# Kernel tuning notes

Measured on AMD Instinct MI355X. Metric: run time of the kernel, lower is better.

Reference implementation:

```python
import jax, jax.numpy as jnp
import numpy as np

M = 768   # num edges
N = 768   # num loops (== M because original tiles image_x with len(edge_x) for both)
C = 256
IMG = 1024
CAT = 3 * C + IMG  # 1792, 'sharing' suffix without '1d'/'noimage'
EPS = 1e-4


def _lin_block(x, W, b):
    # LinearBlock: Linear + ReLU
    return jax.nn.relu(x @ W + b)


def _pred_head(x, W1, b1, W2, b2):
    # Sequential(LinearBlock(256,64), Linear(64,1)) -> sigmoid -> flatten
    return jax.nn.sigmoid(_lin_block(x, W1, b1) @ W2 + b2).reshape(-1)


def setup_inputs() -> dict:
    key = jax.random.key(0)
    ks = jax.random.split(key, 24)
    s = 0.02
    return {
        "edge_x": jax.random.normal(ks[0], (M, C), jnp.float32),
        "loop_x": jax.random.normal(ks[1], (N, C), jnp.float32),
        "image_x": jax.random.normal(ks[2], (1, IMG), jnp.float32),
        "loop_edge_masks": (jax.random.uniform(ks[3], (N, M)) < 0.3).astype(jnp.float32),
        "edge_conflict_mask": (jax.random.uniform(ks[4], (M, M)) < 0.1).astype(jnp.float32),
        "loop_conflict_mask": (jax.random.uniform(ks[5], (N, N)) < 0.1).astype(jnp.float32),
        "loop_masks": jax.random.uniform(ks[6], (N, 64), jnp.float32),      # pass-through only
        "loop_edge_indices": jax.random.randint(ks[7], (N,), 0, M, jnp.int32),  # unused ('1d' off)
        "edge_info": jax.random.normal(ks[8], (M, 4), jnp.float32),         # unused ('1d' off)
        "W_e3": jax.random.normal(ks[9], (CAT, C), jnp.float32) * s,
        "b_e3": jnp.zeros((C,), jnp.float32),
        "W_l3": jax.random.normal(ks[10], (CAT, C), jnp.float32) * s,
        "b_l3": jnp.zeros((C,), jnp.float32),
        "W_ep1": jax.random.normal(ks[11], (C, 64), jnp.float32) * s,
        "b_ep1": jnp.zeros((64,), jnp.float32),
        "W_ep2": jax.random.normal(ks[12], (64, 1), jnp.float32) * s,
        "b_ep2": jnp.zeros((1,), jnp.float32),
        "W_lp1": jax.random.normal(ks[13], (C, 64), jnp.float32) * s,
        "b_lp1": jnp.zeros((64,), jnp.float32),
        "W_lp2": jax.random.normal(ks[14], (64, 1), jnp.float32) * s,
        "b_lp2": jnp.zeros((1,), jnp.float32),
    }


def reference(edge_x, loop_x, image_x, loop_edge_masks, edge_conflict_mask,
              loop_conflict_mask, loop_masks, loop_edge_indices, edge_info,
              W_e3, b_e3, W_l3, b_l3, W_ep1, b_ep1, W_ep2, b_ep2,
              W_lp1, b_lp1, W_lp2, b_lp2):
    # iteration-0 predictions (appended to results in original)
    e0 = _pred_head(edge_x, W_ep1, b_ep1, W_ep2, b_ep2)  # [M]
    l0 = _pred_head(loop_x, W_lp1, b_lp1, W_lp2, b_lp2)  # [N]

    # weights[n, m] = mask * |loop_pred[n] - edge_pred[m]|
    w = loop_edge_masks * jnp.abs(l0[:, None] - e0[None, :])  # [N, M]

    # weighted broadcast sums (einsum == unsqueeze-multiply-sum in the original)
    edge_x_from_loop = jnp.einsum('nm,nc->mc', w, loop_x) \
        / jnp.maximum(w.sum(0), EPS)[:, None]               # [M, C]
    loop_x_from_edge = jnp.einsum('nm,mc->nc', w, edge_x) \
        / jnp.maximum(w.sum(1), EPS)[:, None]               # [N, C]

    # conflict-masked max pooling (materializes [M,M,C]/[N,N,C] like the original)
    edge_x_from_conflict = jnp.max(edge_conflict_mask[:, :, None] * edge_x[None, :, :], axis=1)
    loop_x_from_conflict = jnp.max(loop_conflict_mask[:, :, None] * loop_x[None, :, :], axis=1)

    img_e = jnp.broadcast_to(image_x, (edge_x.shape[0], image_x.shape[1]))
    img_l = jnp.broadcast_to(image_x, (loop_x.shape[0], image_x.shape[1]))

    edge_x2 = _lin_block(jnp.concatenate([edge_x, edge_x_from_loop, edge_x_from_conflict, img_e], axis=-1), W_e3, b_e3)
    loop_x2 = _lin_block(jnp.concatenate([loop_x, loop_x_from_edge, loop_x_from_conflict, img_l], axis=-1), W_l3, b_l3)

    e1 = _pred_head(edge_x2, W_ep1, b_ep1, W_ep2, b_ep2)
    l1 = _pred_head(loop_x2, W_lp1, b_lp1, W_lp2, b_lp2)

    # original returns results=[[e0,l0,masks,loop_masks],[e1,l1,masks,loop_masks]];
    # masks are constant pass-throughs, so we return the predictions concatenated.
    return jnp.concatenate([e0, l0, e1, l1])  # [2*(M+N)] = [3072]
```

## Files before the change

### kernel.cpp

```cpp
#include <hip/hip_runtime.h>
#include <hip/hip_bf16.h>
#include <math.h>

#define MM 768
#define CC 256
#define EPSV 1e-4f

__device__ __forceinline__ float sigmoidf_(float x) { return 1.0f / (1.0f + expf(-x)); }

__global__ __launch_bounds__(256) void k_prep(
    const float* __restrict__ edge_x, const float* __restrict__ loop_x,
    const float* __restrict__ image_x,
    const float* __restrict__ ecm, const float* __restrict__ lcm,
    const float* __restrict__ We3, const float* __restrict__ Wl3,
    const float* __restrict__ Wep1, const float* __restrict__ bep1,
    const float* __restrict__ Wep2, const float* __restrict__ bep2,
    const float* __restrict__ Wlp1, const float* __restrict__ blp1,
    const float* __restrict__ Wlp2, const float* __restrict__ blp2,
    float* __restrict__ out, float* __restrict__ efc, float* __restrict__ lfc,
    float* __restrict__ imgpart)
{
    int bid = blockIdx.x;
    int t   = threadIdx.x;

    if (bid < 1536) {
        __shared__ int   s_cnt;
        __shared__ int   s_idx[MM];
        __shared__ float s_val[MM];
        bool isLoop = bid >= MM;
        int  m      = bid & (MM - 1);
        const float* mask = isLoop ? lcm : ecm;
        const float* x    = isLoop ? loop_x : edge_x;
        float*       o    = isLoop ? lfc : efc;

        if (t == 0) s_cnt = 0;
        __syncthreads();
        int lane = t & 63;
        #pragma unroll
        for (int r = 0; r < 3; ++r) {
            int j = t + r * 256;
            float v = mask[m * MM + j];
            bool nz = (v != 0.0f);
            unsigned long long b = __ballot(nz);
            int prefix = __popcll(b & ((1ull << lane) - 1ull));
            int cntw   = __popcll(b);
            int base = 0;
            if (lane == 0 && cntw) base = atomicAdd(&s_cnt, cntw);
            base = __shfl(base, 0, 64);
            if (nz) { s_idx[base + prefix] = j; s_val[base + prefix] = v; }
        }
        __syncthreads();
        int cnt = s_cnt;
        float init = (cnt < MM) ? 0.0f : -INFINITY;
        float a0 = init, a1 = init, a2 = init, a3 = init;
        int i = 0;
        for (; i + 4 <= cnt; i += 4) {
            a0 = fmaxf(a0, s_val[i + 0] * x[s_idx[i + 0] * CC + t]);
            a1 = fmaxf(a1, s_val[i + 1] * x[s_idx[i + 1] * CC + t]);
            a2 = fmaxf(a2, s_val[i + 2] * x[s_idx[i + 2] * CC + t]);
            a3 = fmaxf(a3, s_val[i + 3] * x[s_idx[i + 3] * CC + t]);
        }
        for (; i < cnt; ++i)
            a0 = fmaxf(a0, s_val[i] * x[s_idx[i] * CC + t]);
        o[m * CC + t] = fmaxf(fmaxf(a0, a1), fmaxf(a2, a3));

    } else if (bid < 1920) {
        int wave = t >> 6, lane = t & 63;
        int row  = (bid - 1536) * 4 + wave;
        const float *x, *W1, *b1, *W2;
        float b2v;
        if (row < MM) { x = edge_x + row * CC;        W1 = Wep1; b1 = bep1; W2 = Wep2; b2v = bep2[0]; }
        else          { x = loop_x + (row - MM) * CC; W1 = Wlp1; b1 = blp1; W2 = Wlp2; b2v = blp2[0]; }

        float a0 = 0.f, a1 = 0.f, a2 = 0.f, a3 = 0.f;
        for (int cc = 0; cc < CC; cc += 4) {
            float4 xv = *reinterpret_cast<const float4*>(x + cc);
            a0 = fmaf(xv.x, W1[(cc + 0) * 64 + lane], a0);
            a1 = fmaf(xv.y, W1[(cc + 1) * 64 + lane], a1);
            a2 = fmaf(xv.z, W1[(cc + 2) * 64 + lane], a2);
            a3 = fmaf(xv.w, W1[(cc + 3) * 64 + lane], a3);
        }
        float h = fmaxf(b1[lane] + ((a0 + a1) + (a2 + a3)), 0.0f);
        float p = h * W2[lane];
        #pragma unroll
        for (int off = 32; off; off >>= 1) p += __shfl_xor(p, off, 64);
        if (lane == 0) out[row] = sigmoidf_(p + b2v);

    } else {
        int sub   = bid - 1920;
        int chunk = sub & 3;
        int head  = sub >> 2;
        const float* W = head ? Wl3 : We3;
        int k0 = chunk * 256;
        float s = 0.0f;
        #pragma unroll 4
        for (int k = 0; k < 256; ++k)
            s = fmaf(image_x[k0 + k], W[(768 + k0 + k) * CC + t], s);
        imgpart[head * 1024 + chunk * 256 + t] = s;
    }
}

__global__ __launch_bounds__(512) void k_bsum(
    const float* __restrict__ lem, const float* __restrict__ edge_x,
    const float* __restrict__ loop_x, const float* __restrict__ pred,
    float* __restrict__ efl, float* __restrict__ lfe)
{
    __shared__ float4 s_wv4[MM];
    __shared__ float  s_pw[8 * 4];
    __shared__ float  s_sum[4];
    float* s_wv = reinterpret_cast<float*>(s_wv4);

    int bid = blockIdx.x;
    int t   = threadIdx.x;
    const float* e0 = pred;
    const float* l0 = pred + MM;

    bool isE = bid < 192;
    int  r0  = (isE ? bid : bid - 192) * 4;
    const float* ownp = isE ? e0 : l0;
    const float* othp = isE ? l0 : e0;

    float own[4];
    #pragma unroll
    for (int i = 0; i < 4; ++i) own[i] = ownp[r0 + i];

    int i_ = t & 3;
    float myown = own[0];
    if (i_ == 1) myown = own[1];
    else if (i_ == 2) myown = own[2];
    else if (i_ == 3) myown = own[3];
    float psum = 0.f;
    #pragma unroll
    for (int k = 0; k < 6; ++k) {
        int idx = t + k * 512;
        int s = idx >> 2;
        float lm = isE ? lem[s * MM + r0 + i_] : lem[(r0 + i_) * MM + s];
        float wv = lm * fabsf(othp[s] - myown);
        s_wv[idx] = wv;
        psum += wv;
    }
    #pragma unroll
    for (int off = 4; off < 64; off <<= 1) psum += __shfl_xor(psum, off, 64);
    int wave = t >> 6, lane = t & 63;
    if (lane < 4) s_pw[wave * 4 + lane] = psum;
    __syncthreads();
    if (t < 4) {
        float s = 0.f;
        #pragma unroll
        for (int w = 0; w < 8; ++w) s += s_pw[w * 4 + t];
        s_sum[t] = fmaxf(s, EPSV);
    }

    const float* xsrc = isE ? loop_x : edge_x;
    int c = t & 255, h = t >> 8;
    float acc0 = 0.f, acc1 = 0.f, acc2 = 0.f, acc3 = 0.f;
    int s0 = h * 384;
    for (int s = s0; s < s0 + 384; s += 4) {
        float4 wa = s_wv4[s + 0];
        float4 wb = s_wv4[s + 1];
        float4 wc = s_wv4[s + 2];
        float4 wd = s_wv4[s + 3];
        float xa = xsrc[(s + 0) * CC + c];
        float xb = xsrc[(s + 1) * CC + c];
        float xc = xsrc[(s + 2) * CC + c];
        float xd = xsrc[(s + 3) * CC + c];
        acc0 = fmaf(wa.x, xa, acc0); acc1 = fmaf(wa.y, xa, acc1);
        acc2 = fmaf(wa.z, xa, acc2); acc3 = fmaf(wa.w, xa, acc3);
        acc0 = fmaf(wb.x, xb, acc0); acc1 = fmaf(wb.y, xb, acc1);
        acc2 = fmaf(wb.z, xb, acc2); acc3 = fmaf(wb.w, xb, acc3);
        acc0 = fmaf(wc.x, xc, acc0); acc1 = fmaf(wc.y, xc, acc1);
        acc2 = fmaf(wc.z, xc, acc2); acc3 = fmaf(wc.w, xc, acc3);
        acc0 = fmaf(wd.x, xd, acc0); acc1 = fmaf(wd.y, xd, acc1);
        acc2 = fmaf(wd.z, xd, acc2); acc3 = fmaf(wd.w, xd, acc3);
    }
    __syncthreads();
    if (h == 1) {
        s_wv[0 * CC + c] = acc0; s_wv[1 * CC + c] = acc1;
        s_wv[2 * CC + c] = acc2; s_wv[3 * CC + c] = acc3;
    }
    __syncthreads();
    if (h == 0) {
        float* outp = isE ? efl : lfe;
        outp[(r0 + 0) * CC + c] = (acc0 + s_wv[0 * CC + c]) / s_sum[0];
        outp[(r0 + 1) * CC + c] = (acc1 + s_wv[1 * CC + c]) / s_sum[1];
        outp[(r0 + 2) * CC + c] = (acc2 + s_wv[2 * CC + c]) / s_sum[2];
        outp[(r0 + 3) * CC + c] = (acc3 + s_wv[3 * CC + c]) / s_sum[3];
    }
}

__global__ __launch_bounds__(512) void k_cat(
    const float* __restrict__ edge_x, const float* __restrict__ loop_x,
    const float* __restrict__ efl, const float* __restrict__ lfe,
    const float* __restrict__ efc, const float* __restrict__ lfc,
    const float* __restrict__ We3, const float* __restrict__ be3,
    const float* __restrict__ Wl3, const float* __restrict__ bl3,
    const float* __restrict__ imgpart,
    const float* __restrict__ Wep1, const float* __restrict__ bep1,
    const float* __restrict__ Wep2, const float* __restrict__ bep2,
    const float* __restrict__ Wlp1, const float* __restrict__ blp1,
    const float* __restrict__ Wlp2, const float* __restrict__ blp2,
    float* __restrict__ out)
{
    __shared__ float s_part[4 * CC];
    __shared__ float s_act[4 * CC];
    __shared__ float s_h[8 * 64];

    int head = blockIdx.y;
    const float* W  = head ? Wl3 : We3;
    const float* b  = head ? bl3 : be3;
    const float* x0 = head ? loop_x : edge_x;
    const float* x1 = head ? lfe : efl;
    const float* x2 = head ? lfc : efc;
    const float* ip = imgpart + head * 1024;

    int m0 = blockIdx.x * 4;
    int t  = threadIdx.x;
    int c  = t & 255, h = t >> 8;

    float acc[4] = {0.f, 0.f, 0.f, 0.f};

    auto accum = [&](const float* src, int ks, int kw, int len) {
        for (int kk = 0; kk < len; kk += 4) {
            float4 xv[4];
            #pragma unroll
            for (int i = 0; i < 4; ++i)
                xv[i] = *reinterpret_cast<const float4*>(src + (m0 + i) * CC + ks + kk);
            #pragma unroll
            for (int j = 0; j < 4; ++j) {
                float wv = W[(kw + kk + j) * CC + c];
                #pragma unroll
                for (int i = 0; i < 4; ++i)
                    acc[i] = fmaf(reinterpret_cast<const float*>(&xv[i])[j], wv, acc[i]);
            }
        }
    };
    if (h == 0) { accum(x0, 0, 0, 256);     accum(x1, 0, 256, 128); }
    else        { accum(x1, 128, 384, 128); accum(x2, 0, 512, 256); }

    if (h == 1) {
        #pragma unroll
        for (int i = 0; i < 4; ++i) s_part[i * CC + c] = acc[i];
    }
    __syncthreads();
    if (h == 0) {
        float bias = b[c] + ip[c] + ip[256 + c] + ip[512 + c] + ip[768 + c];
        #pragma unroll
        for (int i = 0; i < 4; ++i)
            s_act[i * CC + c] = fmaxf(bias + acc[i] + s_part[i * CC + c], 0.0f);
    }
    __syncthreads();

    int wave = t >> 6, lane = t & 63;
    int row = wave >> 1, khalf = wave & 1;
    const float* W1 = head ? Wlp1 : Wep1;
    const float* b1 = head ? blp1 : bep1;
    const float* W2 = head ? Wlp2 : Wep2;
    float b2v       = head ? blp2[0] : bep2[0];
    const float* xr = s_act + row * CC + khalf * 128;

    float a0 = 0.f, a1 = 0.f, a2 = 0.f, a3 = 0.f;
    for (int cc = 0; cc < 128; cc += 4) {
        float4 xv = *reinterpret_cast<const float4*>(xr + cc);
        int kb = khalf * 128 + cc;
        a0 = fmaf(xv.x, W1[(kb + 0) * 64 + lane], a0);
        a1 = fmaf(xv.y, W1[(kb + 1) * 64 + lane], a1);
        a2 = fmaf(xv.z, W1[(kb + 2) * 64 + lane], a2);
        a3 = fmaf(xv.w, W1[(kb + 3) * 64 + lane], a3);
    }
    s_h[wave * 64 + lane] = (a0 + a1) + (a2 + a3);
    __syncthreads();
    if (khalf == 0) {
        float hv = fmaxf(b1[lane] + s_h[wave * 64 + lane] + s_h[(wave + 1) * 64 + lane], 0.0f);
        float p = hv * W2[lane];
        #pragma unroll
        for (int off = 32; off; off >>= 1) p += __shfl_xor(p, off, 64);
        if (lane == 0) out[1536 + head * MM + m0 + row] = sigmoidf_(p + b2v);
    }
}

extern "C" void kernel_launch(void* const* d_in, const int* in_sizes, int n_in,
                              void* d_out, int out_size, void* d_ws, size_t ws_size,
                              hipStream_t stream)
{
    const float* edge_x  = (const float*)d_in[0];
    const float* loop_x  = (const float*)d_in[1];
    const float* image_x = (const float*)d_in[2];
    const float* lem     = (const float*)d_in[3];
    const float* ecm     = (const float*)d_in[4];
    const float* lcm     = (const float*)d_in[5];
    const float* We3  = (const float*)d_in[9];
    const float* be3  = (const float*)d_in[10];
    const float* Wl3  = (const float*)d_in[11];
    const float* bl3  = (const float*)d_in[12];
    const float* Wep1 = (const float*)d_in[13];
    const float* bep1 = (const float*)d_in[14];
    const float* Wep2 = (const float*)d_in[15];
    const float* bep2 = (const float*)d_in[16];
    const float* Wlp1 = (const float*)d_in[17];
    const float* blp1 = (const float*)d_in[18];
    const float* Wlp2 = (const float*)d_in[19];
    const float* blp2 = (const float*)d_in[20];

    float* out = (float*)d_out;
    float* ws  = (float*)d_ws;

    float* imgpart = ws;
    float* efl     = ws + 2048;
    float* lfe     = efl + MM * CC;
    float* efc     = lfe + MM * CC;
    float* lfc     = efc + MM * CC;

    k_prep<<<1928, 256, 0, stream>>>(edge_x, loop_x, image_x, ecm, lcm,
                                     We3, Wl3,
                                     Wep1, bep1, Wep2, bep2,
                                     Wlp1, blp1, Wlp2, blp2,
                                     out, efc, lfc, imgpart);

    k_bsum<<<384, 512, 0, stream>>>(lem, edge_x, loop_x, out, efl, lfe);

    k_cat<<<dim3(192, 2), 512, 0, stream>>>(edge_x, loop_x, efl, lfe, efc, lfc,
                                            We3, be3, Wl3, bl3, imgpart,
                                            Wep1, bep1, Wep2, bep2,
                                            Wlp1, blp1, Wlp2, blp2, out);
}
```

Measured before the change: 169.9 us.

## Split-K the bsum matmul across two blocks and register-tile both GEMM kernels

k_bsum now runs two blocks per 4-row group. Each block recomputes the full weight vector and its normalizer, but accumulates only half of the source rows. It writes a partial, already-normalized result into a separate buffer, and k_cat adds the two partials when it loads them. Both k_bsum and k_cat switch from one output column per thread with split halves to 8 waves, each covering a slice of K, with float4 loads and a 4x4 register tile per thread. The per-wave partials are combined by a shared-memory tree reduction. This aims for better occupancy and vectorized memory access, at the cost of duplicated weight-vector work, extra workspace traffic for the partials, and several extra barriers.

```diff
diff --git a/kernel.cpp b/kernel.cpp
--- a/kernel.cpp
+++ b/kernel.cpp
@@ -103,32 +103,31 @@
 __global__ __launch_bounds__(512) void k_bsum(
     const float* __restrict__ lem, const float* __restrict__ edge_x,
     const float* __restrict__ loop_x, const float* __restrict__ pred,
-    float* __restrict__ efl, float* __restrict__ lfe)
+    float* __restrict__ efl_p0, float* __restrict__ efl_p1,
+    float* __restrict__ lfe_p0, float* __restrict__ lfe_p1)
 {
     __shared__ float4 s_wv4[MM];
     __shared__ float  s_pw[8 * 4];
     __shared__ float  s_sum[4];
+    __shared__ float  s_red[4 * 16 * 64];
     float* s_wv = reinterpret_cast<float*>(s_wv4);
 
-    int bid = blockIdx.x;
-    int t   = threadIdx.x;
+    int bid  = blockIdx.x;
+    int t    = threadIdx.x;
+    int pair = bid >> 1, sh = bid & 1;
     const float* e0 = pred;
     const float* l0 = pred + MM;
 
-    bool isE = bid < 192;
-    int  r0  = (isE ? bid : bid - 192) * 4;
+    bool isE = pair < 192;
+    int  r0  = (isE ? pair : pair - 192) * 4;
     const float* ownp = isE ? e0 : l0;
     const float* othp = isE ? l0 : e0;
 
-    float own[4];
-    #pragma unroll
-    for (int i = 0; i < 4; ++i) own[i] = ownp[r0 + i];
+    float own0 = ownp[r0], own1 = ownp[r0 + 1], own2 = ownp[r0 + 2], own3 = ownp[r0 + 3];
 
     int i_ = t & 3;
-    float myown = own[0];
-    if (i_ == 1) myown = own[1];
-    else if (i_ == 2) myown = own[2];
-    else if (i_ == 3) myown = own[3];
+    float myown = own0;
+    if (i_ == 1) myown = own1; else if (i_ == 2) myown = own2; else if (i_ == 3) myown = own3;
     float psum = 0.f;
     #pragma unroll
     for (int k = 0; k < 6; ++k) {
@@ -152,45 +151,87 @@
     }
 
     const float* xsrc = isE ? loop_x : edge_x;
-    int c = t & 255, h = t >> 8;
-    float acc0 = 0.f, acc1 = 0.f, acc2 = 0.f, acc3 = 0.f;
-    int s0 = h * 384;
-    for (int s = s0; s < s0 + 384; s += 4) {
-        float4 wa = s_wv4[s + 0];
-        float4 wb = s_wv4[s + 1];
-        float4 wc = s_wv4[s + 2];
-        float4 wd = s_wv4[s + 3];
-        float xa = xsrc[(s + 0) * CC + c];
-        float xb = xsrc[(s + 1) * CC + c];
-        float xc = xsrc[(s + 2) * CC + c];
-        float xd = xsrc[(s + 3) * CC + c];
-        acc0 = fmaf(wa.x, xa, acc0); acc1 = fmaf(wa.y, xa, acc1);
-        acc2 = fmaf(wa.z, xa, acc2); acc3 = fmaf(wa.w, xa, acc3);
-        acc0 = fmaf(wb.x, xb, acc0); acc1 = fmaf(wb.y, xb, acc1);
-        acc2 = fmaf(wb.z, xb, acc2); acc3 = fmaf(wb.w, xb, acc3);
-        acc0 = fmaf(wc.x, xc, acc0); acc1 = fmaf(wc.y, xc, acc1);
-        acc2 = fmaf(wc.z, xc, acc2); acc3 = fmaf(wc.w, xc, acc3);
-        acc0 = fmaf(wd.x, xd, acc0); acc1 = fmaf(wd.y, xd, acc1);
-        acc2 = fmaf(wd.z, xd, acc2); acc3 = fmaf(wd.w, xd, acc3);
-    }
-    __syncthreads();
-    if (h == 1) {
-        s_wv[0 * CC + c] = acc0; s_wv[1 * CC + c] = acc1;
-        s_wv[2 * CC + c] = acc2; s_wv[3 * CC + c] = acc3;
-    }
-    __syncthreads();
-    if (h == 0) {
-        float* outp = isE ? efl : lfe;
-        outp[(r0 + 0) * CC + c] = (acc0 + s_wv[0 * CC + c]) / s_sum[0];
-        outp[(r0 + 1) * CC + c] = (acc1 + s_wv[1 * CC + c]) / s_sum[1];
-        outp[(r0 + 2) * CC + c] = (acc2 + s_wv[2 * CC + c]) / s_sum[2];
-        outp[(r0 + 3) * CC + c] = (acc3 + s_wv[3 * CC + c]) / s_sum[3];
+    int s_base = sh * 384 + wave * 48;
+    float acc[4][4];
+    #pragma unroll
+    for (int i = 0; i < 4; ++i)
+        #pragma unroll
+        for (int c = 0; c < 4; ++c) acc[i][c] = 0.f;
+
+    #pragma unroll 4
+    for (int j = 0; j < 48; ++j) {
+        int s = s_base + j;
+        float4 w4 = s_wv4[s];
+        float4 xv = *reinterpret_cast<const float4*>(xsrc + s * CC + lane * 4);
+        acc[0][0] = fmaf(w4.x, xv.x, acc[0][0]); acc[0][1] = fmaf(w4.x, xv.y, acc[0][1]);
+        acc[0][2] = fmaf(w4.x, xv.z, acc[0][2]); acc[0][3] = fmaf(w4.x, xv.w, acc[0][3]);
+        acc[1][0] = fmaf(w4.y, xv.x, acc[1][0]); acc[1][1] = fmaf(w4.y, xv.y, acc[1][1]);
+        acc[1][2] = fmaf(w4.y, xv.z, acc[1][2]); acc[1][3] = fmaf(w4.y, xv.w, acc[1][3]);
+        acc[2][0] = fmaf(w4.z, xv.x, acc[2][0]); acc[2][1] = fmaf(w4.z, xv.y, acc[2][1]);
+        acc[2][2] = fmaf(w4.z, xv.z, acc[2][2]); acc[2][3] = fmaf(w4.z, xv.w, acc[2][3]);
+        acc[3][0] = fmaf(w4.w, xv.x, acc[3][0]); acc[3][1] = fmaf(w4.w, xv.y, acc[3][1]);
+        acc[3][2] = fmaf(w4.w, xv.z, acc[3][2]); acc[3][3] = fmaf(w4.w, xv.w, acc[3][3]);
+    }
+
+    if (wave >= 4) {
+        #pragma unroll
+        for (int i = 0; i < 4; ++i)
+            #pragma unroll
+            for (int c = 0; c < 4; ++c)
+                s_red[(wave - 4) * 1024 + (i * 4 + c) * 64 + lane] = acc[i][c];
+    }
+    __syncthreads();
+    if (wave < 4) {
+        #pragma unroll
+        for (int i = 0; i < 4; ++i)
+            #pragma unroll
+            for (int c = 0; c < 4; ++c)
+                acc[i][c] += s_red[wave * 1024 + (i * 4 + c) * 64 + lane];
+    }
+    __syncthreads();
+    if (wave == 2 || wave == 3) {
+        #pragma unroll
+        for (int i = 0; i < 4; ++i)
+            #pragma unroll
+            for (int c = 0; c < 4; ++c)
+                s_red[(wave - 2) * 1024 + (i * 4 + c) * 64 + lane] = acc[i][c];
+    }
+    __syncthreads();
+    if (wave < 2) {
+        #pragma unroll
+        for (int i = 0; i < 4; ++i)
+            #pragma unroll
+            for (int c = 0; c < 4; ++c)
+                acc[i][c] += s_red[wave * 1024 + (i * 4 + c) * 64 + lane];
+    }
+    __syncthreads();
+    if (wave == 1) {
+        #pragma unroll
+        for (int i = 0; i < 4; ++i)
+            #pragma unroll
+            for (int c = 0; c < 4; ++c)
+                s_red[(i * 4 + c) * 64 + lane] = acc[i][c];
+    }
+    __syncthreads();
+    if (wave == 0) {
+        float* outp = isE ? (sh ? efl_p1 : efl_p0) : (sh ? lfe_p1 : lfe_p0);
+        #pragma unroll
+        for (int i = 0; i < 4; ++i) {
+            float inv = 1.0f / s_sum[i];
+            float4 o;
+            o.x = (acc[i][0] + s_red[(i * 4 + 0) * 64 + lane]) * inv;
+            o.y = (acc[i][1] + s_red[(i * 4 + 1) * 64 + lane]) * inv;
+            o.z = (acc[i][2] + s_red[(i * 4 + 2) * 64 + lane]) * inv;
+            o.w = (acc[i][3] + s_red[(i * 4 + 3) * 64 + lane]) * inv;
+            *reinterpret_cast<float4*>(outp + (r0 + i) * CC + lane * 4) = o;
+        }
     }
 }
 
 __global__ __launch_bounds__(512) void k_cat(
     const float* __restrict__ edge_x, const float* __restrict__ loop_x,
-    const float* __restrict__ efl, const float* __restrict__ lfe,
+    const float* __restrict__ efl_p0, const float* __restrict__ efl_p1,
+    const float* __restrict__ lfe_p0, const float* __restrict__ lfe_p1,
     const float* __restrict__ efc, const float* __restrict__ lfc,
     const float* __restrict__ We3, const float* __restrict__ be3,
     const float* __restrict__ Wl3, const float* __restrict__ bl3,
@@ -201,56 +242,132 @@
     const float* __restrict__ Wlp2, const float* __restrict__ blp2,
     float* __restrict__ out)
 {
-    __shared__ float s_part[4 * CC];
+    __shared__ float s_red[4 * 16 * 64];
     __shared__ float s_act[4 * CC];
     __shared__ float s_h[8 * 64];
 
     int head = blockIdx.y;
-    const float* W  = head ? Wl3 : We3;
-    const float* b  = head ? bl3 : be3;
-    const float* x0 = head ? loop_x : edge_x;
-    const float* x1 = head ? lfe : efl;
-    const float* x2 = head ? lfc : efc;
-    const float* ip = imgpart + head * 1024;
+    const float* W   = head ? Wl3 : We3;
+    const float* b   = head ? bl3 : be3;
+    const float* x0  = head ? loop_x : edge_x;
+    const float* x1a = head ? lfe_p0 : efl_p0;
+    const float* x1b = head ? lfe_p1 : efl_p1;
+    const float* x2  = head ? lfc : efc;
+    const float* ip  = imgpart + head * 1024;
 
     int m0 = blockIdx.x * 4;
     int t  = threadIdx.x;
-    int c  = t & 255, h = t >> 8;
-
-    float acc[4] = {0.f, 0.f, 0.f, 0.f};
-
-    auto accum = [&](const float* src, int ks, int kw, int len) {
-        for (int kk = 0; kk < len; kk += 4) {
-            float4 xv[4];
+    int wave = t >> 6, lane = t & 63;
+
+    float acc[4][4];
+    #pragma unroll
+    for (int i = 0; i < 4; ++i)
+        #pragma unroll
+        for (int c = 0; c < 4; ++c) acc[i][c] = 0.f;
+
+    int k0 = wave * 96;
+    for (int jj = 0; jj < 96; jj += 4) {
+        int k = k0 + jj;
+        float4 xr[4];
+        if (k < 256) {
             #pragma unroll
             for (int i = 0; i < 4; ++i)
-                xv[i] = *reinterpret_cast<const float4*>(src + (m0 + i) * CC + ks + kk);
-            #pragma unroll
-            for (int j = 0; j < 4; ++j) {
-                float wv = W[(kw + kk + j) * CC + c];
-                #pragma unroll
-                for (int i = 0; i < 4; ++i)
-                    acc[i] = fmaf(reinterpret_cast<const float*>(&xv[i])[j], wv, acc[i]);
+                xr[i] = *reinterpret_cast<const float4*>(x0 + (m0 + i) * CC + k);
+        } else if (k < 512) {
+            int kk = k - 256;
+            #pragma unroll
+            for (int i = 0; i < 4; ++i) {
+                float4 a = *reinterpret_cast<const float4*>(x1a + (m0 + i) * CC + kk);
+                float4 bb = *reinterpret_cast<const float4*>(x1b + (m0 + i) * CC + kk);
+                xr[i].x = a.x + bb.x; xr[i].y = a.y + bb.y;
+                xr[i].z = a.z + bb.z; xr[i].w = a.w + bb.w;
             }
-        }
-    };
-    if (h == 0) { accum(x0, 0, 0, 256);     accum(x1, 0, 256, 128); }
-    else        { accum(x1, 128, 384, 128); accum(x2, 0, 512, 256); }
-
-    if (h == 1) {
-        #pragma unroll
-        for (int i = 0; i < 4; ++i) s_part[i * CC + c] = acc[i];
-    }
-    __syncthreads();
-    if (h == 0) {
-        float bias = b[c] + ip[c] + ip[256 + c] + ip[512 + c] + ip[768 + c];
-        #pragma unroll
-        for (int i = 0; i < 4; ++i)
-            s_act[i * CC + c] = fmaxf(bias + acc[i] + s_part[i * CC + c], 0.0f);
-    }
-    __syncthreads();
-
-    int wave = t >> 6, lane = t & 63;
+        } else {
+            int kk = k - 512;
+            #pragma unroll
+            for (int i = 0; i < 4; ++i)
+                xr[i] = *reinterpret_cast<const float4*>(x2 + (m0 + i) * CC + kk);
+        }
+        #pragma unroll
+        for (int j = 0; j < 4; ++j) {
+            float4 wv = *reinterpret_cast<const float4*>(W + (k + j) * CC + lane * 4);
+            float xj0 = reinterpret_cast<const float*>(&xr[0])[j];
+            float xj1 = reinterpret_cast<const float*>(&xr[1])[j];
+            float xj2 = reinterpret_cast<const float*>(&xr[2])[j];
+            float xj3 = reinterpret_cast<const float*>(&xr[3])[j];
+            acc[0][0] = fmaf(xj0, wv.x, acc[0][0]); acc[0][1] = fmaf(xj0, wv.y, acc[0][1]);
+            acc[0][2] = fmaf(xj0, wv.z, acc[0][2]); acc[0][3] = fmaf(xj0, wv.w, acc[0][3]);
+            acc[1][0] = fmaf(xj1, wv.x, acc[1][0]); acc[1][1] = fmaf(xj1, wv.y, acc[1][1]);
+            acc[1][2] = fmaf(xj1, wv.z, acc[1][2]); acc[1][3] = fmaf(xj1, wv.w, acc[1][3]);
+            acc[2][0] = fmaf(xj2, wv.x, acc[2][0]); acc[2][1] = fmaf(xj2, wv.y, acc[2][1]);
+            acc[2][2] = fmaf(xj2, wv.z, acc[2][2]); acc[2][3] = fmaf(xj2, wv.w, acc[2][3]);
+            acc[3][0] = fmaf(xj3, wv.x, acc[3][0]); acc[3][1] = fmaf(xj3, wv.y, acc[3][1]);
+            acc[3][2] = fmaf(xj3, wv.z, acc[3][2]); acc[3][3] = fmaf(xj3, wv.w, acc[3][3]);
+        }
+    }
+
+    if (wave >= 4) {
+        #pragma unroll
+        for (int i = 0; i < 4; ++i)
+            #pragma unroll
+            for (int c = 0; c < 4; ++c)
+                s_red[(wave - 4) * 1024 + (i * 4 + c) * 64 + lane] = acc[i][c];
+    }
+    __syncthreads();
+    if (wave < 4) {
+        #pragma unroll
+        for (int i = 0; i < 4; ++i)
+            #pragma unroll
+            for (int c = 0; c < 4; ++c)
+                acc[i][c] += s_red[wave * 1024 + (i * 4 + c) * 64 + lane];
+    }
+    __syncthreads();
+    if (wave == 2 || wave == 3) {
+        #pragma unroll
+        for (int i = 0; i < 4; ++i)
+            #pragma unroll
+            for (int c = 0; c < 4; ++c)
+                s_red[(wave - 2) * 1024 + (i * 4 + c) * 64 + lane] = acc[i][c];
+    }
+    __syncthreads();
+    if (wave < 2) {
+        #pragma unroll
+        for (int i = 0; i < 4; ++i)
+            #pragma unroll
+            for (int c = 0; c < 4; ++c)
+                acc[i][c] += s_red[wave * 1024 + (i * 4 + c) * 64 + lane];
+    }
+    __syncthreads();
+    if (wave == 1) {
+        #pragma unroll
+        for (int i = 0; i < 4; ++i)
+            #pragma unroll
+            for (int c = 0; c < 4; ++c)
+                s_red[(i * 4 + c) * 64 + lane] = acc[i][c];
+    }
+    __syncthreads();
+    if (wave == 0) {
+        float4 b4  = *reinterpret_cast<const float4*>(b + lane * 4);
+        float4 i0  = *reinterpret_cast<const float4*>(ip + lane * 4);
+        float4 i1  = *reinterpret_cast<const float4*>(ip + 256 + lane * 4);
+        float4 i2  = *reinterpret_cast<const float4*>(ip + 512 + lane * 4);
+        float4 i3  = *reinterpret_cast<const float4*>(ip + 768 + lane * 4);
+        float bias[4] = { b4.x + i0.x + i1.x + i2.x + i3.x,
+                          b4.y + i0.y + i1.y + i2.y + i3.y,
+                          b4.z + i0.z + i1.z + i2.z + i3.z,
+                          b4.w + i0.w + i1.w + i2.w + i3.w };
+        #pragma unroll
+        for (int i = 0; i < 4; ++i) {
+            float4 o;
+            o.x = fmaxf(acc[i][0] + s_red[(i * 4 + 0) * 64 + lane] + bias[0], 0.f);
+            o.y = fmaxf(acc[i][1] + s_red[(i * 4 + 1) * 64 + lane] + bias[1], 0.f);
+            o.z = fmaxf(acc[i][2] + s_red[(i * 4 + 2) * 64 + lane] + bias[2], 0.f);
+            o.w = fmaxf(acc[i][3] + s_red[(i * 4 + 3) * 64 + lane] + bias[3], 0.f);
+            *reinterpret_cast<float4*>(s_act + i * CC + lane * 4) = o;
+        }
+    }
+    __syncthreads();
+
     int row = wave >> 1, khalf = wave & 1;
     const float* W1 = head ? Wlp1 : Wep1;
     const float* b1 = head ? blp1 : bep1;
@@ -305,9 +422,11 @@
     float* ws  = (float*)d_ws;
 
     float* imgpart = ws;
-    float* efl     = ws + 2048;
-    float* lfe     = efl + MM * CC;
-    float* efc     = lfe + MM * CC;
+    float* efl_p0  = ws + 2048;
+    float* efl_p1  = efl_p0 + MM * CC;
+    float* lfe_p0  = efl_p1 + MM * CC;
+    float* lfe_p1  = lfe_p0 + MM * CC;
+    float* efc     = lfe_p1 + MM * CC;
     float* lfc     = efc + MM * CC;
 
     k_prep<<<1928, 256, 0, stream>>>(edge_x, loop_x, image_x, ecm, lcm,
@@ -316,9 +435,12 @@
                                      Wlp1, blp1, Wlp2, blp2,
                                      out, efc, lfc, imgpart);
 
-    k_bsum<<<384, 512, 0, stream>>>(lem, edge_x, loop_x, out, efl, lfe);
-
-    k_cat<<<dim3(192, 2), 512, 0, stream>>>(edge_x, loop_x, efl, lfe, efc, lfc,
+    k_bsum<<<768, 512, 0, stream>>>(lem, edge_x, loop_x, out,
+                                    efl_p0, efl_p1, lfe_p0, lfe_p1);
+
+    k_cat<<<dim3(192, 2), 512, 0, stream>>>(edge_x, loop_x,
+                                            efl_p0, efl_p1, lfe_p0, lfe_p1,
+                                            efc, lfc,
                                             We3, be3, Wl3, bl3, imgpart,
                                             Wep1, bep1, Wep2, bep2,
                                             Wlp1, blp1, Wlp2, blp2, out);
```

Result: no change. 170.1 us (+0.2%).
